# Kernel tuning notes

Measured on AMD Instinct MI355X. Metric: run time of the kernel, lower is better.

Reference implementation:

```python
import jax, jax.numpy as jnp
import numpy as np

HEADS = 12
HEAD_DIM = 64
WINDOW = 65  # must be odd
EMBED = 768
B, L = 1, 2048


def setup_inputs() -> dict:
    key = jax.random.key(0)
    k1, k2, k3 = jax.random.split(key, 3)
    x = jax.random.normal(k1, (B, L, EMBED), dtype=jnp.float32)
    w_qkv = jax.random.normal(k2, (EMBED, 3 * HEADS * HEAD_DIM), dtype=jnp.float32) * 0.02
    w_out = jax.random.normal(k3, (HEADS * HEAD_DIM, EMBED), dtype=jnp.float32) * 0.02
    b_out = jnp.zeros((EMBED,), dtype=jnp.float32)
    return {"x": x, "w_qkv": w_qkv, "w_out": w_out, "b_out": b_out}


def reference(x, w_qkv, w_out, b_out):
    b, l, _ = x.shape
    pad = WINDOW // 2
    # qkv projection (no bias), reshape to [B, L, H, 3*Dh], split as in TF code
    qkv = jnp.einsum('ble,ef->blf', x, w_qkv).reshape(b, l, HEADS, 3 * HEAD_DIM)
    q = qkv[..., :HEAD_DIM]                      # [B, L, H, Dh]
    k = qkv[..., HEAD_DIM:2 * HEAD_DIM]
    v = qkv[..., 2 * HEAD_DIM:]
    # zero-pad along sequence (matches tf.pad; padded positions participate in softmax)
    k_pad = jnp.pad(k, ((0, 0), (pad, pad), (0, 0), (0, 0)))  # [B, L+2p, H, Dh]
    v_pad = jnp.pad(v, ((0, 0), (pad, pad), (0, 0), (0, 0)))
    # sliding windows via a single gather: [B, L, W, H, Dh]
    idx = jnp.arange(l)[:, None] + jnp.arange(WINDOW)[None, :]
    k_win = k_pad[:, idx]
    v_win = v_pad[:, idx]
    score = jnp.einsum('blhd,blwhd->blhw', q, k_win) / jnp.sqrt(
        jnp.asarray(HEAD_DIM, dtype=x.dtype))
    weights = jax.nn.softmax(score, axis=-1)      # [B, L, H, W]
    out = jnp.einsum('blhw,blwhd->blhd', weights, v_win)
    out = out.reshape(b, l, HEADS * HEAD_DIM)
    return jnp.einsum('blf,fe->ble', out, w_out) + b_out
```

## Files before the change

kernel.cpp:

```cpp
#include <hip/hip_runtime.h>
#include <hip/hip_bf16.h>

#define HEADS 12
#define HD 64
#define PADW 32
#define EMBED 768
#define LSEQ 2048
#define QKV_N (3 * HEADS * HD)
#define LPAD (LSEQ + 64)

typedef short short8 __attribute__((ext_vector_type(8)));
typedef short short4v __attribute__((ext_vector_type(4)));
typedef float f32x4 __attribute__((ext_vector_type(4)));

__device__ short g_xb[LSEQ * EMBED];
__device__ short g_wqkvT[QKV_N * EMBED];
__device__ short g_woutT[EMBED * EMBED];
__device__ short g_qkvb[LSEQ * QKV_N];
__device__ short g_vT[HEADS * HD * LPAD];
__device__ short g_attnb[LSEQ * EMBED];

__device__ __forceinline__ short f2bf(float f) {
  unsigned x = __builtin_bit_cast(unsigned, f);
  x += 0x7fffu + ((x >> 16) & 1u);
  return (short)(x >> 16);
}

#define GLB(p) ((const __attribute__((address_space(1))) void*)(p))
#define LDS(p) ((__attribute__((address_space(3))) void*)(p))

#define PREP_A 1536
#define PREP_B 1728
#define PREP_C 576
#define PREP_D 24

__global__ __launch_bounds__(256) void prep(
    const float* __restrict__ x, const float* __restrict__ w_qkv,
    const float* __restrict__ w_out, short* __restrict__ xb,
    short* __restrict__ wqkvT, short* __restrict__ woutT,
    short* __restrict__ vT) {
  __shared__ float T[32][33];
  const int b = blockIdx.x, tid = threadIdx.x;
  if (b < PREP_A) {
    int i = b * 256 + tid;
    float4 v = ((const float4*)x)[i];
    short4v o;
    o[0] = f2bf(v.x); o[1] = f2bf(v.y); o[2] = f2bf(v.z); o[3] = f2bf(v.w);
    ((short4v*)xb)[i] = o;
  } else if (b < PREP_A + PREP_B + PREP_C) {
    const float* W; short* WT; int N, bx, by;
    if (b < PREP_A + PREP_B) {
      int t = b - PREP_A; W = w_qkv; WT = wqkvT; N = QKV_N; bx = t % 72; by = t / 72;
    } else {
      int t = b - PREP_A - PREP_B; W = w_out; WT = woutT; N = EMBED; bx = t % 24; by = t / 24;
    }
    const int K = EMBED;
    int tx = tid & 31, ty = tid >> 5;
    int n0 = bx * 32, k0 = by * 32;
#pragma unroll
    for (int p = 0; p < 4; ++p)
      T[ty + p * 8][tx] = W[(size_t)(k0 + ty + p * 8) * N + n0 + tx];
    __syncthreads();
#pragma unroll
    for (int p = 0; p < 4; ++p)
      WT[(size_t)(n0 + ty + p * 8) * K + k0 + tx] = f2bf(T[tx][ty + p * 8]);
  } else {
    int j = (b - PREP_A - PREP_B - PREP_C) * 256 + tid;
    int hd = j >> 3, side = (j >> 2) & 1, off = (j & 3) * 8;
    short8 z = {};
    *(short8*)&vT[(size_t)hd * LPAD + side * 2080 + off] = z;
  }
}

template <int BM, int BN, bool OUT_BF16, bool FUSE_VT>
__global__ __launch_bounds__(256) void gemm_pipe(
    const short* __restrict__ A, const short* __restrict__ Bt,
    const float* __restrict__ bias, void* __restrict__ Cv,
    short* __restrict__ vT, int M, int N, int K) {
  constexpr int MT = BM / 32, NT = BN / 32;
  constexpr int ACH = BM / 64, BCH = BN / 64;
  constexpr int SI = ACH + BCH;
  constexpr int BUF = (BM + BN) * 32;
  constexpr int EPI = OUT_BF16 ? BM * (BN + 16) : BM * (BN + 8) * 2;
  constexpr int LDSZ = (3 * BUF > EPI) ? 3 * BUF : EPI;
  __shared__ __align__(16) short lds_s[LDSZ];

  const int tid = threadIdx.x;
  const int wv = tid >> 6, lane = tid & 63;
  const int wm = wv >> 1, wn = wv & 1;
  const int lanelo = lane & 15, quad = lane >> 4;
  const int m0 = blockIdx.y * BM, n0 = blockIdx.x * BN;
  const int srow = lane >> 2, schk = lane & 3;

  f32x4 acc[MT][NT] = {};

  auto stage = [&](int j, int buf) {
    short* Ab = lds_s + buf * BUF;
    short* Bb = Ab + BM * 32;
    const int k0 = j * 32;
#pragma unroll
    for (int c = 0; c < ACH; ++c) {
      int chunk = wv * ACH + c;
      const short* ga = A + (size_t)(m0 + chunk * 16 + srow) * K + k0 + schk * 8;
      __builtin_amdgcn_global_load_lds(GLB(ga), LDS(&Ab[chunk * 16 * 32]), 16, 0, 0);
    }
#pragma unroll
    for (int c = 0; c < BCH; ++c) {
      int chunk = wv * BCH + c;
      const short* gb = Bt + (size_t)(n0 + chunk * 16 + srow) * K + k0 + schk * 8;
      __builtin_amdgcn_global_load_lds(GLB(gb), LDS(&Bb[chunk * 16 * 32]), 16, 0, 0);
    }
  };

  auto compute = [&](int buf) {
    short* Ab = lds_s + buf * BUF;
    short* Bb = Ab + BM * 32;
    short8 af[MT], bfr[NT];
#pragma unroll
    for (int mt = 0; mt < MT; ++mt)
      af[mt] = *(const short8*)&Ab[(wm * (MT * 16) + mt * 16 + lanelo) * 32 + quad * 8];
#pragma unroll
    for (int nt = 0; nt < NT; ++nt)
      bfr[nt] = *(const short8*)&Bb[(wn * (NT * 16) + nt * 16 + lanelo) * 32 + quad * 8];
    asm volatile("s_waitcnt lgkmcnt(0)" ::: "memory");
#pragma unroll
    for (int mt = 0; mt < MT; ++mt)
#pragma unroll
      for (int nt = 0; nt < NT; ++nt)
        acc[mt][nt] = __builtin_amdgcn_mfma_f32_16x16x32_bf16(af[mt], bfr[nt], acc[mt][nt], 0, 0, 0);
  };

  const int steps = K / 32;
  stage(0, 0);
  stage(1, 1);
  int cur = 0;
  for (int j = 0; j < steps - 1; ++j) {
    if constexpr (SI == 2)      asm volatile("s_waitcnt vmcnt(2)" ::: "memory");
    else if constexpr (SI == 3) asm volatile("s_waitcnt vmcnt(3)" ::: "memory");
    else                        asm volatile("s_waitcnt vmcnt(4)" ::: "memory");
    asm volatile("s_barrier" ::: "memory");
    if (j + 2 < steps) {
      int b2 = cur + 2; if (b2 >= 3) b2 -= 3;
      stage(j + 2, b2);
    }
    compute(cur);
    ++cur; if (cur == 3) cur = 0;
  }
  asm volatile("s_waitcnt vmcnt(0)" ::: "memory");
  asm volatile("s_barrier" ::: "memory");
  compute(cur);

  if (FUSE_VT) {
#pragma unroll
    for (int nt = 0; nt < NT; ++nt) {
      int c0 = n0 + wn * (NT * 16) + nt * 16;
      if ((c0 % 192) >= 128) {
        int h = c0 / 192, d0 = (c0 % 192) - 128;
#pragma unroll
        for (int mt = 0; mt < MT; ++mt) {
          int d = d0 + lanelo;
          int row0 = m0 + wm * (MT * 16) + mt * 16 + quad * 4;
          short4v o;
#pragma unroll
          for (int r = 0; r < 4; ++r) o[r] = f2bf(acc[mt][nt][r]);
          *(short4v*)&vT[(size_t)(h * 64 + d) * LPAD + PADW + row0] = o;
        }
      }
    }
  }

  __syncthreads();
  if (OUT_BF16) {
    constexpr int ST = BN + 16;
#pragma unroll
    for (int mt = 0; mt < MT; ++mt)
#pragma unroll
      for (int nt = 0; nt < NT; ++nt) {
        int rloc = wm * (MT * 16) + mt * 16 + quad * 4;
        int cloc = wn * (NT * 16) + nt * 16 + lanelo;
#pragma unroll
        for (int r = 0; r < 4; ++r)
          lds_s[(rloc + r) * ST + cloc] = f2bf(acc[mt][nt][r]);
      }
    __syncthreads();
    constexpr int TPR = BN / 8, RPP = 256 / TPR;
    short* Cc = (short*)Cv;
#pragma unroll
    for (int rp = 0; rp < BM; rp += RPP) {
      int row = rp + tid / TPR, seg = tid % TPR;
      short8 vv = *(const short8*)&lds_s[row * ST + seg * 8];
      *(short8*)&Cc[(size_t)(m0 + row) * N + n0 + seg * 8] = vv;
    }
  } else {
    constexpr int ST = BN + 8;
    float* fl = (float*)lds_s;
#pragma unroll
    for (int mt = 0; mt < MT; ++mt)
#pragma unroll
      for (int nt = 0; nt < NT; ++nt) {
        int rloc = wm * (MT * 16) + mt * 16 + quad * 4;
        int cloc = wn * (NT * 16) + nt * 16 + lanelo;
#pragma unroll
        for (int r = 0; r < 4; ++r)
          fl[(rloc + r) * ST + cloc] = acc[mt][nt][r];
      }
    __syncthreads();
    constexpr int TPR = BN / 4, RPP = 256 / TPR;
    float* Cc = (float*)Cv;
#pragma unroll
    for (int rp = 0; rp < BM; rp += RPP) {
      int row = rp + tid / TPR, seg = tid % TPR;
      float4 vv = *(const float4*)&fl[row * ST + seg * 4];
      float4 bb = *(const float4*)&bias[n0 + seg * 4];
      vv.x += bb.x; vv.y += bb.y; vv.z += bb.z; vv.w += bb.w;
      *(float4*)&Cc[(size_t)(m0 + row) * N + n0 + seg * 4] = vv;
    }
  }
}

__global__ __launch_bounds__(256) void attn_mfma(
    const short* __restrict__ qkvb, const short* __restrict__ vT,
    short* __restrict__ attnb) {
  const int blk = blockIdx.x;
  const int h = blk % HEADS;
  const int l0 = (blk / HEADS) * 64;
  const int sb = l0 - PADW;

  const int tid = threadIdx.x;
  const int wv = tid >> 6, lane = tid & 63;
  const int lanelo = lane & 15, quad = lane >> 4;
  const int qoff = h * 192, koff = h * 192 + 64;

  __shared__ __align__(16) short P_lds[64 * 136];

  const short* qp = qkvb + (size_t)(l0 + wv * 16 + lanelo) * QKV_N + qoff;
  short8 aq0 = *(const short8*)(qp + quad * 8);
  short8 aq1 = *(const short8*)(qp + 32 + quad * 8);

  f32x4 sacc[8] = {};
#pragma unroll
  for (int nt = 0; nt < 8; ++nt) {
    int gl = sb + nt * 16 + lanelo;
    short8 bk0 = {}, bk1 = {};
    if ((unsigned)gl < (unsigned)LSEQ) {
      const short* kp = qkvb + (size_t)gl * QKV_N + koff;
      bk0 = *(const short8*)(kp + quad * 8);
      bk1 = *(const short8*)(kp + 32 + quad * 8);
    }
    sacc[nt] = __builtin_amdgcn_mfma_f32_16x16x32_bf16(aq0, bk0, sacc[nt], 0, 0, 0);
    sacc[nt] = __builtin_amdgcn_mfma_f32_16x16x32_bf16(aq1, bk1, sacc[nt], 0, 0, 0);
  }

  short8 bv[4][4];
#pragma unroll
  for (int ks = 0; ks < 4; ++ks) {
    int lp = l0 + ks * 32 + quad * 8;
#pragma unroll
    for (int nt = 0; nt < 4; ++nt) {
      int d = nt * 16 + lanelo;
      bv[ks][nt] = *(const short8*)&vT[((size_t)h * 64 + d) * LPAD + lp];
    }
  }

  float rsum[4] = {0.f, 0.f, 0.f, 0.f};
#pragma unroll
  for (int nt = 0; nt < 8; ++nt)
#pragma unroll
    for (int r = 0; r < 4; ++r) {
      int li = wv * 16 + quad * 4 + r;
      int widx = nt * 16 + lanelo - li;
      float s = (widx >= 0 && widx <= 64) ? sacc[nt][r] * 0.125f : -1e30f;
      float p = __expf(s);
      sacc[nt][r] = p;
      rsum[r] += p;
    }
#pragma unroll
  for (int r = 0; r < 4; ++r) {
#pragma unroll
    for (int off = 1; off < 16; off <<= 1)
      rsum[r] += __shfl_xor(rsum[r], off);
    rsum[r] = 1.f / rsum[r];
  }
#pragma unroll
  for (int nt = 0; nt < 8; ++nt)
#pragma unroll
    for (int r = 0; r < 4; ++r) {
      int row = wv * 16 + quad * 4 + r;
      P_lds[row * 136 + nt * 16 + lanelo] = f2bf(sacc[nt][r] * rsum[r]);
    }
  __syncthreads();

  f32x4 oacc[4] = {};
#pragma unroll
  for (int ks = 0; ks < 4; ++ks) {
    short8 ap = *(const short8*)&P_lds[(wv * 16 + lanelo) * 136 + ks * 32 + quad * 8];
#pragma unroll
    for (int nt = 0; nt < 4; ++nt)
      oacc[nt] = __builtin_amdgcn_mfma_f32_16x16x32_bf16(ap, bv[ks][nt], oacc[nt], 0, 0, 0);
  }

  __syncthreads();
#pragma unroll
  for (int nt = 0; nt < 4; ++nt)
#pragma unroll
    for (int r = 0; r < 4; ++r) {
      int row = wv * 16 + quad * 4 + r;
      P_lds[row * 80 + nt * 16 + lanelo] = f2bf(oacc[nt][r]);
    }
  __syncthreads();
#pragma unroll
  for (int rp = 0; rp < 64; rp += 32) {
    int row = rp + tid / 8, seg = tid % 8;
    short8 vv = *(const short8*)&P_lds[row * 80 + seg * 8];
    *(short8*)&attnb[(size_t)(l0 + row) * EMBED + h * 64 + seg * 8] = vv;
  }
}

extern "C" void kernel_launch(void* const* d_in, const int* in_sizes, int n_in,
                              void* d_out, int out_size, void* d_ws, size_t ws_size,
                              hipStream_t stream) {
  const float* x     = (const float*)d_in[0];
  const float* w_qkv = (const float*)d_in[1];
  const float* w_out = (const float*)d_in[2];
  const float* b_out = (const float*)d_in[3];
  float* out = (float*)d_out;

  short *xb, *wqkvT, *woutT, *qkvb, *vT, *attnb;
  hipGetSymbolAddress((void**)&xb,    HIP_SYMBOL(g_xb));
  hipGetSymbolAddress((void**)&wqkvT, HIP_SYMBOL(g_wqkvT));
  hipGetSymbolAddress((void**)&woutT, HIP_SYMBOL(g_woutT));
  hipGetSymbolAddress((void**)&qkvb,  HIP_SYMBOL(g_qkvb));
  hipGetSymbolAddress((void**)&vT,    HIP_SYMBOL(g_vT));
  hipGetSymbolAddress((void**)&attnb, HIP_SYMBOL(g_attnb));

  prep<<<PREP_A + PREP_B + PREP_C + PREP_D, 256, 0, stream>>>(
      x, w_qkv, w_out, xb, wqkvT, woutT, vT);

  gemm_pipe<128, 128, true, true><<<dim3(QKV_N / 128, LSEQ / 128), 256, 0, stream>>>(
      xb, wqkvT, nullptr, qkvb, vT, LSEQ, QKV_N, EMBED);

  attn_mfma<<<(LSEQ / 64) * HEADS, 256, 0, stream>>>(qkvb, vT, attnb);

  gemm_pipe<64, 64, false, false><<<dim3(EMBED / 64, LSEQ / 64), 256, 0, stream>>>(
      attnb, woutT, b_out, out, nullptr, LSEQ, EMBED, EMBED);
}
```

Measured before the change: 117.4 us.

## Fuse all four stages into one persistent kernel with software grid barriers

```diff
diff --git a/kernel.cpp b/kernel.cpp
--- a/kernel.cpp
+++ b/kernel.cpp
@@ -20,6 +20,9 @@
 __device__ short g_vT[HEADS * HD * LPAD];
 __device__ short g_attnb[LSEQ * EMBED];
 
+__device__ unsigned g_bar_cnt = 0;
+__device__ unsigned g_bar_gen = 0;
+
 __device__ __forceinline__ short f2bf(float f) {
   unsigned x = __builtin_bit_cast(unsigned, f);
   x += 0x7fffu + ((x >> 16) & 1u);
@@ -29,18 +32,40 @@
 #define GLB(p) ((const __attribute__((address_space(1))) void*)(p))
 #define LDS(p) ((__attribute__((address_space(3))) void*)(p))
 
+__device__ __forceinline__ void grid_barrier() {
+  __syncthreads();
+  if (threadIdx.x == 0) {
+    __threadfence();
+    unsigned gen = __hip_atomic_load(&g_bar_gen, __ATOMIC_SEQ_CST,
+                                     __HIP_MEMORY_SCOPE_AGENT);
+    unsigned t = __hip_atomic_fetch_add(&g_bar_cnt, 1u, __ATOMIC_SEQ_CST,
+                                        __HIP_MEMORY_SCOPE_AGENT);
+    if (t == gridDim.x - 1) {
+      __hip_atomic_store(&g_bar_cnt, 0u, __ATOMIC_RELAXED,
+                         __HIP_MEMORY_SCOPE_AGENT);
+      __hip_atomic_fetch_add(&g_bar_gen, 1u, __ATOMIC_RELEASE,
+                             __HIP_MEMORY_SCOPE_AGENT);
+    } else {
+      while (__hip_atomic_load(&g_bar_gen, __ATOMIC_ACQUIRE,
+                               __HIP_MEMORY_SCOPE_AGENT) == gen)
+        __builtin_amdgcn_s_sleep(2);
+    }
+    __threadfence();
+  }
+  __syncthreads();
+}
+
 #define PREP_A 1536
 #define PREP_B 1728
 #define PREP_C 576
 #define PREP_D 24
-
-__global__ __launch_bounds__(256) void prep(
-    const float* __restrict__ x, const float* __restrict__ w_qkv,
+#define PREP_TOT (PREP_A + PREP_B + PREP_C + PREP_D)
+
+__device__ __forceinline__ void prep_unit(
+    int b, int tid, const float* __restrict__ x, const float* __restrict__ w_qkv,
     const float* __restrict__ w_out, short* __restrict__ xb,
     short* __restrict__ wqkvT, short* __restrict__ woutT,
-    short* __restrict__ vT) {
-  __shared__ float T[32][33];
-  const int b = blockIdx.x, tid = threadIdx.x;
+    short* __restrict__ vT, short* lds) {
   if (b < PREP_A) {
     int i = b * 256 + tid;
     float4 v = ((const float4*)x)[i];
@@ -48,6 +73,7 @@
     o[0] = f2bf(v.x); o[1] = f2bf(v.y); o[2] = f2bf(v.z); o[3] = f2bf(v.w);
     ((short4v*)xb)[i] = o;
   } else if (b < PREP_A + PREP_B + PREP_C) {
+    float (*T)[33] = (float(*)[33])lds;
     const float* W; short* WT; int N, bx, by;
     if (b < PREP_A + PREP_B) {
       int t = b - PREP_A; W = w_qkv; WT = wqkvT; N = QKV_N; bx = t % 72; by = t / 72;
@@ -64,6 +90,7 @@
 #pragma unroll
     for (int p = 0; p < 4; ++p)
       WT[(size_t)(n0 + ty + p * 8) * K + k0 + tx] = f2bf(T[tx][ty + p * 8]);
+    __syncthreads();
   } else {
     int j = (b - PREP_A - PREP_B - PREP_C) * 256 + tid;
     int hd = j >> 3, side = (j >> 2) & 1, off = (j & 3) * 8;
@@ -73,23 +100,20 @@
 }
 
 template <int BM, int BN, bool OUT_BF16, bool FUSE_VT>
-__global__ __launch_bounds__(256) void gemm_pipe(
+__device__ __forceinline__ void gemm_tile(
+    int bx, int by, int tid,
     const short* __restrict__ A, const short* __restrict__ Bt,
     const float* __restrict__ bias, void* __restrict__ Cv,
-    short* __restrict__ vT, int M, int N, int K) {
+    short* __restrict__ vT, int M, int N, int K, short* lds_s) {
   constexpr int MT = BM / 32, NT = BN / 32;
   constexpr int ACH = BM / 64, BCH = BN / 64;
   constexpr int SI = ACH + BCH;
   constexpr int BUF = (BM + BN) * 32;
-  constexpr int EPI = OUT_BF16 ? BM * (BN + 16) : BM * (BN + 8) * 2;
-  constexpr int LDSZ = (3 * BUF > EPI) ? 3 * BUF : EPI;
-  __shared__ __align__(16) short lds_s[LDSZ];
-
-  const int tid = threadIdx.x;
+
   const int wv = tid >> 6, lane = tid & 63;
   const int wm = wv >> 1, wn = wv & 1;
   const int lanelo = lane & 15, quad = lane >> 4;
-  const int m0 = blockIdx.y * BM, n0 = blockIdx.x * BN;
+  const int m0 = by * BM, n0 = bx * BN;
   const int srow = lane >> 2, schk = lane & 3;
 
   f32x4 acc[MT][NT] = {};
@@ -191,6 +215,7 @@
       short8 vv = *(const short8*)&lds_s[row * ST + seg * 8];
       *(short8*)&Cc[(size_t)(m0 + row) * N + n0 + seg * 8] = vv;
     }
+    __syncthreads();
   } else {
     constexpr int ST = BN + 8;
     float* fl = (float*)lds_s;
@@ -215,23 +240,20 @@
       vv.x += bb.x; vv.y += bb.y; vv.z += bb.z; vv.w += bb.w;
       *(float4*)&Cc[(size_t)(m0 + row) * N + n0 + seg * 4] = vv;
     }
-  }
-}
-
-__global__ __launch_bounds__(256) void attn_mfma(
-    const short* __restrict__ qkvb, const short* __restrict__ vT,
-    short* __restrict__ attnb) {
-  const int blk = blockIdx.x;
+    __syncthreads();
+  }
+}
+
+__device__ __forceinline__ void attn_tile(
+    int blk, int tid, const short* __restrict__ qkvb,
+    const short* __restrict__ vT, short* __restrict__ attnb, short* P_lds) {
   const int h = blk % HEADS;
   const int l0 = (blk / HEADS) * 64;
   const int sb = l0 - PADW;
 
-  const int tid = threadIdx.x;
   const int wv = tid >> 6, lane = tid & 63;
   const int lanelo = lane & 15, quad = lane >> 4;
   const int qoff = h * 192, koff = h * 192 + 64;
-
-  __shared__ __align__(16) short P_lds[64 * 136];
 
   const short* qp = qkvb + (size_t)(l0 + wv * 16 + lanelo) * QKV_N + qoff;
   short8 aq0 = *(const short8*)(qp + quad * 8);
@@ -314,6 +336,71 @@
     short8 vv = *(const short8*)&P_lds[row * 80 + seg * 8];
     *(short8*)&attnb[(size_t)(l0 + row) * EMBED + h * 64 + seg * 8] = vv;
   }
+  __syncthreads();
+}
+
+#define FUSED_GRID 512
+#define GEMM1_TILES 288
+#define ATTN_TILES 384
+#define GEMM2_TILES 384
+
+__global__ __launch_bounds__(256, 2) void fused_all(
+    const float* __restrict__ x, const float* __restrict__ w_qkv,
+    const float* __restrict__ w_out, const float* __restrict__ b_out,
+    float* __restrict__ out,
+    short* __restrict__ xb, short* __restrict__ wqkvT,
+    short* __restrict__ woutT, short* __restrict__ qkvb,
+    short* __restrict__ vT, short* __restrict__ attnb) {
+  __shared__ __align__(16) short lds[3 * (128 + 128) * 32];
+  const int tid = threadIdx.x;
+  const int bid = blockIdx.x;
+
+  for (int b = bid; b < PREP_TOT; b += FUSED_GRID)
+    prep_unit(b, tid, x, w_qkv, w_out, xb, wqkvT, woutT, vT, lds);
+  grid_barrier();
+
+  if (bid < GEMM1_TILES)
+    gemm_tile<128, 128, true, true>(bid % 18, bid / 18, tid, xb, wqkvT,
+                                    nullptr, qkvb, vT, LSEQ, QKV_N, EMBED, lds);
+  grid_barrier();
+
+  if (bid < ATTN_TILES)
+    attn_tile(bid, tid, qkvb, vT, attnb, lds);
+  grid_barrier();
+
+  if (bid < GEMM2_TILES)
+    gemm_tile<64, 64, false, false>(bid % 12, bid / 12, tid, attnb, woutT,
+                                    b_out, out, nullptr, LSEQ, EMBED, EMBED, lds);
+}
+
+__global__ __launch_bounds__(256) void prep(
+    const float* __restrict__ x, const float* __restrict__ w_qkv,
+    const float* __restrict__ w_out, short* __restrict__ xb,
+    short* __restrict__ wqkvT, short* __restrict__ woutT,
+    short* __restrict__ vT) {
+  __shared__ __align__(16) float T[32][33];
+  prep_unit(blockIdx.x, threadIdx.x, x, w_qkv, w_out, xb, wqkvT, woutT, vT,
+            (short*)T);
+}
+
+template <int BM, int BN, bool OUT_BF16, bool FUSE_VT>
+__global__ __launch_bounds__(256) void gemm_pipe(
+    const short* __restrict__ A, const short* __restrict__ Bt,
+    const float* __restrict__ bias, void* __restrict__ Cv,
+    short* __restrict__ vT, int M, int N, int K) {
+  constexpr int BUF = (BM + BN) * 32;
+  constexpr int EPI = OUT_BF16 ? BM * (BN + 16) : BM * (BN + 8) * 2;
+  constexpr int LDSZ = (3 * BUF > EPI) ? 3 * BUF : EPI;
+  __shared__ __align__(16) short lds_s[LDSZ];
+  gemm_tile<BM, BN, OUT_BF16, FUSE_VT>(blockIdx.x, blockIdx.y, threadIdx.x,
+                                       A, Bt, bias, Cv, vT, M, N, K, lds_s);
+}
+
+__global__ __launch_bounds__(256) void attn_mfma(
+    const short* __restrict__ qkvb, const short* __restrict__ vT,
+    short* __restrict__ attnb) {
+  __shared__ __align__(16) short P_lds[64 * 136];
+  attn_tile(blockIdx.x, threadIdx.x, qkvb, vT, attnb, P_lds);
 }
 
 extern "C" void kernel_launch(void* const* d_in, const int* in_sizes, int n_in,
@@ -326,21 +413,26 @@
   float* out = (float*)d_out;
 
   short *xb, *wqkvT, *woutT, *qkvb, *vT, *attnb;
-  hipGetSymbolAddress((void**)&xb,    HIP_SYMBOL(g_xb));
-  hipGetSymbolAddress((void**)&wqkvT, HIP_SYMBOL(g_wqkvT));
-  hipGetSymbolAddress((void**)&woutT, HIP_SYMBOL(g_woutT));
-  hipGetSymbolAddress((void**)&qkvb,  HIP_SYMBOL(g_qkvb));
-  hipGetSymbolAddress((void**)&vT,    HIP_SYMBOL(g_vT));
-  hipGetSymbolAddress((void**)&attnb, HIP_SYMBOL(g_attnb));
-
-  prep<<<PREP_A + PREP_B + PREP_C + PREP_D, 256, 0, stream>>>(
-      x, w_qkv, w_out, xb, wqkvT, woutT, vT);
-
+  (void)hipGetSymbolAddress((void**)&xb,    HIP_SYMBOL(g_xb));
+  (void)hipGetSymbolAddress((void**)&wqkvT, HIP_SYMBOL(g_wqkvT));
+  (void)hipGetSymbolAddress((void**)&woutT, HIP_SYMBOL(g_woutT));
+  (void)hipGetSymbolAddress((void**)&qkvb,  HIP_SYMBOL(g_qkvb));
+  (void)hipGetSymbolAddress((void**)&vT,    HIP_SYMBOL(g_vT));
+  (void)hipGetSymbolAddress((void**)&attnb, HIP_SYMBOL(g_attnb));
+
+  int nb = 0;
+  hipError_t qe = hipOccupancyMaxActiveBlocksPerMultiprocessor(
+      &nb, reinterpret_cast<const void*>(&fused_all), 256, 0);
+  if (qe == hipSuccess && nb >= 2) {
+    fused_all<<<FUSED_GRID, 256, 0, stream>>>(
+        x, w_qkv, w_out, b_out, out, xb, wqkvT, woutT, qkvb, vT, attnb);
+    return;
+  }
+
+  prep<<<PREP_TOT, 256, 0, stream>>>(x, w_qkv, w_out, xb, wqkvT, woutT, vT);
   gemm_pipe<128, 128, true, true><<<dim3(QKV_N / 128, LSEQ / 128), 256, 0, stream>>>(
       xb, wqkvT, nullptr, qkvb, vT, LSEQ, QKV_N, EMBED);
-
   attn_mfma<<<(LSEQ / 64) * HEADS, 256, 0, stream>>>(qkvb, vT, attnb);
-
   gemm_pipe<64, 64, false, false><<<dim3(EMBED / 64, LSEQ / 64), 256, 0, stream>>>(
       attnb, woutT, b_out, out, nullptr, LSEQ, EMBED, EMBED);
 }
```

After: 117.0 us. About the same (-0.4%).
